# Performance work log

Hardware: AMD Instinct MI355X
Metric: run time of the kernel (lower is better)

Reference implementation:

```python
import jax, jax.numpy as jnp
import numpy as np

B, M, L, E, H = 64, 1, 4096, 4096, 64  # note: module requires M==1 and B==H
DK = E // H
EPS = 1e-8  # torch CosineSimilarity eps


def setup_inputs() -> dict:
    key = jax.random.key(0)
    ks = jax.random.split(key, 11)
    s_in = 1.0 / np.sqrt(L)
    s_e = 1.0 / np.sqrt(E)
    u = lambda k, shape, s: jax.random.uniform(k, shape, jnp.float32, -s, s)
    return {
        "q": jax.random.normal(ks[0], (B, M, L), jnp.float32),
        "k": jax.random.normal(ks[1], (B, M, L), jnp.float32),
        "v": jax.random.normal(ks[2], (B, M, L), jnp.float32),
        "Wq": u(ks[3], (L, E), s_in), "bq": u(ks[4], (E,), s_in),
        "Wk": u(ks[5], (L, E), s_in), "bk": u(ks[6], (E,), s_in),
        "Wv": u(ks[7], (L, E), s_in), "bv": u(ks[8], (E,), s_in),
        "Wo": u(ks[9], (E, E), s_e), "bo": u(ks[10], (E,), s_e),
    }


def reference(q, k, v, Wq, bq, Wk, bk, Wv, bv, Wo, bo):
    b = q.shape[0]
    # M == 1, so (B,1,L) -> (B,L); project and split into heads: (B,H,DK)
    qh = (q[:, 0, :] @ Wq + bq).reshape(b, H, DK)
    kh = (k[:, 0, :] @ Wk + bk).reshape(b, H, DK)
    vh = (v[:, 0, :] @ Wv + bv).reshape(b, H, DK)
    # cosine similarity over dk (dim=2): (B,H)
    num = jnp.sum(qh * kh, axis=-1)
    den = jnp.maximum(
        jnp.sqrt(jnp.sum(qh * qh, axis=-1)) * jnp.sqrt(jnp.sum(kh * kh, axis=-1)),
        EPS,
    )
    dist = jax.nn.softmax(num / den, axis=-1)  # softmax over heads, (B,H)
    # dropout is identity in eval mode.
    # torch.matmul((B,H), (B,H,DK)) broadcasts to (B, B, DK): out[i,j] = dist[j] @ v[i]
    attn = jnp.einsum('jh,bhd->bjd', dist, vh)  # (B, B, DK), valid since B == H
    attn = attn.reshape(b, E)
    return attn @ Wo + bo  # (B, E)
```

## Files before the change

kernel.cpp:

```cpp
#include <hip/hip_runtime.h>
#include <hip/hip_bf16.h>
#include <math.h>


#define TL 4096
#define NB 64
#define KSQ 4
#define KSO 8

typedef float f32x4 __attribute__((ext_vector_type(4)));
typedef short bf16x8 __attribute__((ext_vector_type(8)));
typedef unsigned int uint32;
typedef unsigned short u16;

union B8 { uint32 u[4]; bf16x8 v; };

#define GLOAD_LDS(g, l)                                                        \
  __builtin_amdgcn_global_load_lds(                                           \
      (const __attribute__((address_space(1))) void*)(g),                     \
      (__attribute__((address_space(3))) void*)(l), 16, 0, 0)

#define WAITCNT(n) asm volatile("s_waitcnt vmcnt(" #n ")" ::: "memory")

__device__ __forceinline__ void split_pair(float f0, float f1, uint32& hp,
                                           uint32& lp) {
  uint32 u0 = __float_as_uint(f0), u1 = __float_as_uint(f1);
  hp = (u0 >> 16) | (u1 & 0xffff0000u);
  float l0 = f0 - __uint_as_float(u0 & 0xffff0000u);
  float l1 = f1 - __uint_as_float(u1 & 0xffff0000u);
  lp = (__float_as_uint(l0) >> 16) | (__float_as_uint(l1) & 0xffff0000u);
}


struct Ptrs3 { const float* X[3]; u16* H[3]; u16* L[3]; };

__global__ __launch_bounds__(256) void prep_kernel(Ptrs3 p) {
  const int m = blockIdx.y;
  const int fid = blockIdx.x * 256 + threadIdx.x;
  const int lane = fid & 63, fi = fid >> 6;
  const int t = fi >> 2, rt = fi & 3;
  const int row = rt * 16 + (lane & 15);
  const int k0 = t * 32 + (lane >> 4) * 8;
  const float* src = p.X[m] + (size_t)row * TL + k0;
  const float4 f0 = *reinterpret_cast<const float4*>(src);
  const float4 f1 = *reinterpret_cast<const float4*>(src + 4);
  uint4 h, l;
  split_pair(f0.x, f0.y, h.x, l.x);
  split_pair(f0.z, f0.w, h.y, l.y);
  split_pair(f1.x, f1.y, h.z, l.z);
  split_pair(f1.z, f1.w, h.w, l.w);
  *reinterpret_cast<uint4*>(p.H[m] + (size_t)fid * 8) = h;
  *reinterpret_cast<uint4*>(p.L[m] + (size_t)fid * 8) = l;
}

struct GemmArgs {
  const u16* Ah[3];
  const u16* Al[3];
  const float* W[3];
  float* P[3];
};

template <int KSplit, int NMat, int CB>
__global__ __launch_bounds__(512, 2) void mfma_gemm(GemmArgs ga) {
  constexpr int KR = TL / KSplit;
  constexpr int NT = KR / 32;
  constexpr int NCG = TL / CB;
  constexpr int NWG = NMat * KSplit * NCG;
  constexpr int BSZ = CB * 128;
  constexpr int TSZ = BSZ + 8192;
  constexpr int NBG = CB / 64;
  constexpr int LPR = CB / 4;
  constexpr int SUB = CB / 128;
  static_assert(NWG % 8 == 0, "xcd swizzle needs NWG%8==0");
  static_assert(NT >= 3, "pipeline needs >=3 tiles");
  __shared__ __align__(16) char sb[3 * TSZ];

  const int tid = threadIdx.x;
  const int lane = tid & 63;
  const int w = tid >> 6;
  const int l15 = lane & 15, kg = lane >> 4;

  const int swz = (blockIdx.x & 7) * (NWG / 8) + (blockIdx.x >> 3);
  const int mat = swz / (KSplit * NCG);
  const int r = swz % (KSplit * NCG);
  const int ks = r / NCG;
  const int cg = r % NCG;
  const int k0 = ks * KR;
  const int tg0 = ks * NT;
  const int cg0 = cg * CB;

  const float* Wm = ga.W[mat];
  const u16* Agh = ga.Ah[mat];
  const u16* Agl = ga.Al[mat];

  const u16* Asrc0 = (w < 4 ? Agh : Agl) + (size_t)(w & 3) * 512 + lane * 8;
  const int adst = BSZ + (w < 4 ? 0 : 4096) + (w & 3) * 1024;

  auto STAGE = [&](char* buf, int t) {
    const int kb = k0 + t * 32;
#pragma unroll
    for (int i = 0; i < NBG; ++i) {
      const int gl = w * NBG + i;
      const float* gsrc = Wm + (size_t)(kb + gl * (64 / LPR) + lane / LPR) * TL +
                          cg0 + (lane % LPR) * 4;
      GLOAD_LDS(gsrc, buf + gl * 1024);
    }
    GLOAD_LDS(Asrc0 + (size_t)(tg0 + t) * 2048, buf + adst);
  };

  f32x4 acc[SUB][4] = {};

  auto COMPUTE = [&](const char* buf) {
    const float* Bf = (const float*)buf;
    const char* Ahb = buf + BSZ;
    const char* Alb = buf + BSZ + 4096;
    bf16x8 ah[4], al[4];
#pragma unroll
    for (int rt = 0; rt < 4; ++rt) {
      ah[rt] = *(const bf16x8*)(Ahb + rt * 1024 + lane * 16);
      al[rt] = *(const bf16x8*)(Alb + rt * 1024 + lane * 16);
    }
#pragma unroll
    for (int c2 = 0; c2 < SUB; ++c2) {
      const int wcol = w * (CB / 8) + c2 * 16;
      float f[8];
#pragma unroll
      for (int e = 0; e < 8; ++e) f[e] = Bf[(kg * 8 + e) * CB + wcol + l15];
      B8 bh, bl;
#pragma unroll
      for (int e = 0; e < 4; ++e)
        split_pair(f[2 * e], f[2 * e + 1], bh.u[e], bl.u[e]);
#pragma unroll
      for (int rt = 0; rt < 4; ++rt) {
        acc[c2][rt] = __builtin_amdgcn_mfma_f32_16x16x32_bf16(ah[rt], bh.v, acc[c2][rt], 0, 0, 0);
        acc[c2][rt] = __builtin_amdgcn_mfma_f32_16x16x32_bf16(ah[rt], bl.v, acc[c2][rt], 0, 0, 0);
        acc[c2][rt] = __builtin_amdgcn_mfma_f32_16x16x32_bf16(al[rt], bh.v, acc[c2][rt], 0, 0, 0);
      }
    }
  };

  char* cur = sb;
  char* nxt = sb + TSZ;
  char* stg = sb + 2 * TSZ;
  STAGE(cur, 0);
  STAGE(nxt, 1);

#pragma unroll 1
  for (int t = 0; t < NT; ++t) {
    if (t + 2 < NT) {
      STAGE(stg, t + 2);
      if constexpr (NBG == 4) WAITCNT(10); else WAITCNT(6);
    } else if (t + 2 == NT) {
      if constexpr (NBG == 4) WAITCNT(5); else WAITCNT(3);
    } else {
      WAITCNT(0);
    }
    __builtin_amdgcn_s_barrier();
    COMPUTE(cur);
    __builtin_amdgcn_s_barrier();
    char* tmp = cur; cur = nxt; nxt = stg; stg = tmp;
  }

  float* Pp = ga.P[mat] + ((size_t)ks * NB) * TL + cg0 + w * (CB / 8) + l15;
#pragma unroll
  for (int c2 = 0; c2 < SUB; ++c2)
#pragma unroll
    for (int rt = 0; rt < 4; ++rt)
#pragma unroll
      for (int j = 0; j < 4; ++j)
        Pp[(size_t)(rt * 16 + kg * 4 + j) * TL + c2 * 16] = acc[c2][rt][j];
}

__global__ __launch_bounds__(64) void dist_kernel(
    const float* __restrict__ Pq, const float* __restrict__ Pk,
    const float* __restrict__ bq, const float* __restrict__ bk,
    float* __restrict__ dist) {
  const int b = blockIdx.x;
  const int h = threadIdx.x;
  float num = 0.f, qq = 0.f, kk = 0.f;
#pragma unroll
  for (int d = 0; d < 64; d += 4) {
    f32x4 qv = *(const f32x4*)&bq[h * 64 + d];
    f32x4 kv = *(const f32x4*)&bk[h * 64 + d];
#pragma unroll
    for (int s = 0; s < KSQ; ++s) {
      qv += *(const f32x4*)&Pq[((size_t)s * NB + b) * TL + h * 64 + d];
      kv += *(const f32x4*)&Pk[((size_t)s * NB + b) * TL + h * 64 + d];
    }
#pragma unroll
    for (int e = 0; e < 4; ++e) {
      num += qv[e] * kv[e];
      qq += qv[e] * qv[e];
      kk += kv[e] * kv[e];
    }
  }
  const float den = fmaxf(sqrtf(qq) * sqrtf(kk), 1e-8f);
  float s = num / den;
  float m = s;
#pragma unroll
  for (int off = 32; off; off >>= 1) m = fmaxf(m, __shfl_xor(m, off));
  const float e = expf(s - m);
  float sum = e;
#pragma unroll
  for (int off = 32; off; off >>= 1) sum += __shfl_xor(sum, off);
  dist[b * 64 + h] = e / sum;
}

__global__ __launch_bounds__(256) void attn_kernel(
    const float* __restrict__ Pv, const float* __restrict__ bv,
    const float* __restrict__ dist, u16* __restrict__ Ah,
    u16* __restrict__ Al) {
  const int i = blockIdx.x;
  __shared__ float vrow[TL];
  __shared__ float ds[NB * NB];
  const int tid = threadIdx.x;
#pragma unroll
  for (int f = tid; f < 1024; f += 256) {
    f32x4 v = *(const f32x4*)&bv[f * 4];
#pragma unroll
    for (int s = 0; s < KSQ; ++s)
      v += *(const f32x4*)&Pv[((size_t)s * NB + i) * TL + f * 4];
    *reinterpret_cast<f32x4*>(&vrow[f * 4]) = v;
    *reinterpret_cast<f32x4*>(&ds[f * 4]) =
        *reinterpret_cast<const f32x4*>(&dist[f * 4]);
  }
  __syncthreads();
  const int rt = i >> 4, l15r = i & 15;
#pragma unroll
  for (int s = 0; s < 16; ++s) {
    const int c = tid + 256 * s;
    const int j = c >> 6, d = c & 63;
    float sum = 0.f;
#pragma unroll
    for (int h = 0; h < 64; ++h) sum += ds[j * 64 + h] * vrow[h * 64 + d];
    const uint32 u = __float_as_uint(sum);
    const float lo = sum - __uint_as_float(u & 0xffff0000u);
    const uint32 off =
        (((uint32)(c >> 5) * 4 + rt) * 64 + ((c >> 3) & 3) * 16 + l15r) * 8 +
        (c & 7);
    Ah[off] = (u16)(u >> 16);
    Al[off] = (u16)(__float_as_uint(lo) >> 16);
  }
}

__global__ __launch_bounds__(256) void reduce_kernel(
    const float* __restrict__ Po, const float* __restrict__ bo,
    float* __restrict__ out) {
  const int idx = (blockIdx.x * 256 + threadIdx.x) * 4;
  f32x4 v = *(const f32x4*)&bo[idx & (TL - 1)];
#pragma unroll
  for (int s = 0; s < KSO; ++s)
    v += *(const f32x4*)&Po[(size_t)s * NB * TL + idx];
  *reinterpret_cast<f32x4*>(&out[idx]) = v;
}

extern "C" void kernel_launch(void* const* d_in, const int* in_sizes, int n_in,
                              void* d_out, int out_size, void* d_ws,
                              size_t ws_size, hipStream_t stream) {
  const float* q  = (const float*)d_in[0];
  const float* k  = (const float*)d_in[1];
  const float* v  = (const float*)d_in[2];
  const float* Wq = (const float*)d_in[3];
  const float* bq = (const float*)d_in[4];
  const float* Wk = (const float*)d_in[5];
  const float* bk = (const float*)d_in[6];
  const float* Wv = (const float*)d_in[7];
  const float* bv = (const float*)d_in[8];
  const float* Wo = (const float*)d_in[9];
  const float* bo = (const float*)d_in[10];
  float* out = (float*)d_out;

  char* ws = (char*)d_ws;
  const size_t HB = 512u * 1024u;
  u16* qAh = (u16*)(ws + 0 * HB);
  u16* qAl = (u16*)(ws + 1 * HB);
  u16* kAh = (u16*)(ws + 2 * HB);
  u16* kAl = (u16*)(ws + 3 * HB);
  u16* vAh = (u16*)(ws + 4 * HB);
  u16* vAl = (u16*)(ws + 5 * HB);
  u16* aAh = (u16*)(ws + 6 * HB);
  u16* aAl = (u16*)(ws + 7 * HB);
  float* Pq = (float*)(ws + (4u << 20));
  float* Pk = (float*)(ws + (8u << 20));
  float* Pv = (float*)(ws + (12u << 20));
  float* Po = Pq;
  float* dist = (float*)(ws + (16u << 20));

  Ptrs3 p3;
  p3.X[0] = q; p3.X[1] = k; p3.X[2] = v;
  p3.H[0] = qAh; p3.H[1] = kAh; p3.H[2] = vAh;
  p3.L[0] = qAl; p3.L[1] = kAl; p3.L[2] = vAl;
  prep_kernel<<<dim3(128, 3), 256, 0, stream>>>(p3);

  GemmArgs gq;
  gq.Ah[0] = qAh; gq.Ah[1] = kAh; gq.Ah[2] = vAh;
  gq.Al[0] = qAl; gq.Al[1] = kAl; gq.Al[2] = vAl;
  gq.W[0] = Wq; gq.W[1] = Wk; gq.W[2] = Wv;
  gq.P[0] = Pq; gq.P[1] = Pk; gq.P[2] = Pv;
  mfma_gemm<KSQ, 3, 256><<<3 * KSQ * 16, 512, 0, stream>>>(gq);

  dist_kernel<<<NB, 64, 0, stream>>>(Pq, Pk, bq, bk, dist);

  attn_kernel<<<NB, 256, 0, stream>>>(Pv, bv, dist, aAh, aAl);

  GemmArgs go;
  go.Ah[0] = aAh; go.Ah[1] = aAh; go.Ah[2] = aAh;
  go.Al[0] = aAl; go.Al[1] = aAl; go.Al[2] = aAl;
  go.W[0] = Wo; go.W[1] = Wo; go.W[2] = Wo;
  go.P[0] = Po; go.P[1] = Po; go.P[2] = Po;
  mfma_gemm<KSO, 1, 128><<<KSO * 32, 512, 0, stream>>>(go);

  reduce_kernel<<<256, 256, 0, stream>>>(Po, bo, out);
}
```

Baseline: 105.4 us.

## Restructure split-bf16 GEMM to 4-wave blocks with swizzled LDS and double buffering

Shrinks the GEMM workgroup from 8 to 4 waves and halves the column tile, so 128-column QKV tiles and 64-column output tiles now run with higher target occupancy. The pipeline drops from three LDS buffers to two, and the weight tile is stored with an XOR column swizzle to avoid LDS bank conflicts. When the workspace is large enough, the QKV projection uses an 8-way K split instead of 4, which gives more blocks but makes the dist and attn kernels reduce twice as many partials. The trade-off is less prefetch depth and more partial-sum traffic, in exchange for better parallelism and fewer LDS conflicts.

```diff
diff --git a/kernel.cpp b/kernel.cpp
--- a/kernel.cpp
+++ b/kernel.cpp
@@ -5,7 +5,6 @@
 
 #define TL 4096
 #define NB 64
-#define KSQ 4
 #define KSO 8
 
 typedef float f32x4 __attribute__((ext_vector_type(4)));
@@ -60,20 +59,21 @@
   float* P[3];
 };
 
-template <int KSplit, int NMat, int CB>
-__global__ __launch_bounds__(512, 2) void mfma_gemm(GemmArgs ga) {
+template <int KSplit, int NMat, int CB, int OCC>
+__global__ __launch_bounds__(256, OCC) void mfma_gemm(GemmArgs ga) {
   constexpr int KR = TL / KSplit;
   constexpr int NT = KR / 32;
   constexpr int NCG = TL / CB;
   constexpr int NWG = NMat * KSplit * NCG;
   constexpr int BSZ = CB * 128;
   constexpr int TSZ = BSZ + 8192;
-  constexpr int NBG = CB / 64;
+  constexpr int NBG = CB / 32;
+  constexpr int RPG = 256 / CB;
   constexpr int LPR = CB / 4;
-  constexpr int SUB = CB / 128;
+  constexpr int SUB = CB / 64;
+  constexpr int G = NBG + 2;
   static_assert(NWG % 8 == 0, "xcd swizzle needs NWG%8==0");
-  static_assert(NT >= 3, "pipeline needs >=3 tiles");
-  __shared__ __align__(16) char sb[3 * TSZ];
+  __shared__ __align__(16) char sb[2 * TSZ];
 
   const int tid = threadIdx.x;
   const int lane = tid & 63;
@@ -93,19 +93,18 @@
   const u16* Agh = ga.Ah[mat];
   const u16* Agl = ga.Al[mat];
 
-  const u16* Asrc0 = (w < 4 ? Agh : Agl) + (size_t)(w & 3) * 512 + lane * 8;
-  const int adst = BSZ + (w < 4 ? 0 : 4096) + (w & 3) * 1024;
-
   auto STAGE = [&](char* buf, int t) {
     const int kb = k0 + t * 32;
 #pragma unroll
     for (int i = 0; i < NBG; ++i) {
       const int gl = w * NBG + i;
-      const float* gsrc = Wm + (size_t)(kb + gl * (64 / LPR) + lane / LPR) * TL +
-                          cg0 + (lane % LPR) * 4;
-      GLOAD_LDS(gsrc, buf + gl * 1024);
-    }
-    GLOAD_LDS(Asrc0 + (size_t)(tg0 + t) * 2048, buf + adst);
+      const int row = gl * RPG + lane / LPR;
+      const int c = ((lane % LPR) * 4) ^ (((row >> 3) & 3) << 3);
+      GLOAD_LDS(Wm + (size_t)(kb + row) * TL + cg0 + c, buf + gl * 1024);
+    }
+    const size_t aoff = ((size_t)(tg0 + t) * 4 + w) * 512 + lane * 8;
+    GLOAD_LDS(Agh + aoff, buf + BSZ + w * 1024);
+    GLOAD_LDS(Agl + aoff, buf + BSZ + 4096 + w * 1024);
   };
 
   f32x4 acc[SUB][4] = {};
@@ -122,10 +121,10 @@
     }
 #pragma unroll
     for (int c2 = 0; c2 < SUB; ++c2) {
-      const int wcol = w * (CB / 8) + c2 * 16;
+      const int colx = ((w * SUB + c2) * 16 + l15) ^ (kg << 3);
       float f[8];
 #pragma unroll
-      for (int e = 0; e < 8; ++e) f[e] = Bf[(kg * 8 + e) * CB + wcol + l15];
+      for (int e = 0; e < 8; ++e) f[e] = Bf[(kg * 8 + e) * CB + colx];
       B8 bh, bl;
 #pragma unroll
       for (int e = 0; e < 4; ++e)
@@ -140,28 +139,24 @@
   };
 
   char* cur = sb;
-  char* nxt = sb + TSZ;
-  char* stg = sb + 2 * TSZ;
+  char* oth = sb + TSZ;
   STAGE(cur, 0);
-  STAGE(nxt, 1);
 
 #pragma unroll 1
   for (int t = 0; t < NT; ++t) {
-    if (t + 2 < NT) {
-      STAGE(stg, t + 2);
-      if constexpr (NBG == 4) WAITCNT(10); else WAITCNT(6);
-    } else if (t + 2 == NT) {
-      if constexpr (NBG == 4) WAITCNT(5); else WAITCNT(3);
+    if (t + 1 < NT) {
+      STAGE(oth, t + 1);
+      if constexpr (G == 6) WAITCNT(6); else WAITCNT(4);
     } else {
       WAITCNT(0);
     }
     __builtin_amdgcn_s_barrier();
     COMPUTE(cur);
     __builtin_amdgcn_s_barrier();
-    char* tmp = cur; cur = nxt; nxt = stg; stg = tmp;
+    char* tmp = cur; cur = oth; oth = tmp;
   }
 
-  float* Pp = ga.P[mat] + ((size_t)ks * NB) * TL + cg0 + w * (CB / 8) + l15;
+  float* Pp = ga.P[mat] + ((size_t)ks * NB) * TL + cg0 + w * SUB * 16 + l15;
 #pragma unroll
   for (int c2 = 0; c2 < SUB; ++c2)
 #pragma unroll
@@ -174,7 +169,7 @@
 __global__ __launch_bounds__(64) void dist_kernel(
     const float* __restrict__ Pq, const float* __restrict__ Pk,
     const float* __restrict__ bq, const float* __restrict__ bk,
-    float* __restrict__ dist) {
+    float* __restrict__ dist, int nks) {
   const int b = blockIdx.x;
   const int h = threadIdx.x;
   float num = 0.f, qq = 0.f, kk = 0.f;
@@ -182,8 +177,7 @@
   for (int d = 0; d < 64; d += 4) {
     f32x4 qv = *(const f32x4*)&bq[h * 64 + d];
     f32x4 kv = *(const f32x4*)&bk[h * 64 + d];
-#pragma unroll
-    for (int s = 0; s < KSQ; ++s) {
+    for (int s = 0; s < nks; ++s) {
       qv += *(const f32x4*)&Pq[((size_t)s * NB + b) * TL + h * 64 + d];
       kv += *(const f32x4*)&Pk[((size_t)s * NB + b) * TL + h * 64 + d];
     }
@@ -209,7 +203,7 @@
 __global__ __launch_bounds__(256) void attn_kernel(
     const float* __restrict__ Pv, const float* __restrict__ bv,
     const float* __restrict__ dist, u16* __restrict__ Ah,
-    u16* __restrict__ Al) {
+    u16* __restrict__ Al, int nks) {
   const int i = blockIdx.x;
   __shared__ float vrow[TL];
   __shared__ float ds[NB * NB];
@@ -217,8 +211,7 @@
 #pragma unroll
   for (int f = tid; f < 1024; f += 256) {
     f32x4 v = *(const f32x4*)&bv[f * 4];
-#pragma unroll
-    for (int s = 0; s < KSQ; ++s)
+    for (int s = 0; s < nks; ++s)
       v += *(const f32x4*)&Pv[((size_t)s * NB + i) * TL + f * 4];
     *reinterpret_cast<f32x4*>(&vrow[f * 4]) = v;
     *reinterpret_cast<f32x4*>(&ds[f * 4]) =
@@ -280,11 +273,13 @@
   u16* vAl = (u16*)(ws + 5 * HB);
   u16* aAh = (u16*)(ws + 6 * HB);
   u16* aAl = (u16*)(ws + 7 * HB);
-  float* Pq = (float*)(ws + (4u << 20));
-  float* Pk = (float*)(ws + (8u << 20));
-  float* Pv = (float*)(ws + (12u << 20));
+
+  const bool big = ws_size >= ((size_t)30 << 20);
+  float* Pq = (float*)(ws + ((size_t)4 << 20));
+  float* Pk = (float*)(ws + ((size_t)(big ? 12 : 8) << 20));
+  float* Pv = (float*)(ws + ((size_t)(big ? 20 : 12) << 20));
+  float* dist = (float*)(ws + ((size_t)(big ? 28 : 16) << 20));
   float* Po = Pq;
-  float* dist = (float*)(ws + (16u << 20));
 
   Ptrs3 p3;
   p3.X[0] = q; p3.X[1] = k; p3.X[2] = v;
@@ -297,18 +292,21 @@
   gq.Al[0] = qAl; gq.Al[1] = kAl; gq.Al[2] = vAl;
   gq.W[0] = Wq; gq.W[1] = Wk; gq.W[2] = Wv;
   gq.P[0] = Pq; gq.P[1] = Pk; gq.P[2] = Pv;
-  mfma_gemm<KSQ, 3, 256><<<3 * KSQ * 16, 512, 0, stream>>>(gq);
-
-  dist_kernel<<<NB, 64, 0, stream>>>(Pq, Pk, bq, bk, dist);
-
-  attn_kernel<<<NB, 256, 0, stream>>>(Pv, bv, dist, aAh, aAl);
+  if (big)
+    mfma_gemm<8, 3, 128, 3><<<768, 256, 0, stream>>>(gq);
+  else
+    mfma_gemm<4, 3, 128, 3><<<384, 256, 0, stream>>>(gq);
+
+  dist_kernel<<<NB, 64, 0, stream>>>(Pq, Pk, bq, bk, dist, big ? 8 : 4);
+
+  attn_kernel<<<NB, 256, 0, stream>>>(Pv, bv, dist, aAh, aAl, big ? 8 : 4);
 
   GemmArgs go;
   go.Ah[0] = aAh; go.Ah[1] = aAh; go.Ah[2] = aAh;
   go.Al[0] = aAl; go.Al[1] = aAl; go.Al[2] = aAl;
   go.W[0] = Wo; go.W[1] = Wo; go.W[2] = Wo;
   go.P[0] = Po; go.P[1] = Po; go.P[2] = Po;
-  mfma_gemm<KSO, 1, 128><<<KSO * 32, 512, 0, stream>>>(go);
+  mfma_gemm<KSO, 1, 64, 2><<<512, 256, 0, stream>>>(go);
 
   reduce_kernel<<<256, 256, 0, stream>>>(Po, bo, out);
 }
```

New measurement: 130.4 us. 1.24x slower.
